# Performance work log

Hardware: AMD Instinct MI355X
Metric: run time of the kernel (lower is better)

Reference implementation:

```python
import jax, jax.numpy as jnp
import numpy as np

N_NODES = 50000
N_EDGES = 800000
IN_NODE = 16
IN_EDGE = 8
HID = 128
N_LAYERS = 4
LN_EPS = 1e-5


def setup_inputs() -> dict:
    key = jax.random.key(0)
    ks = jax.random.split(key, 16)
    s = lambda k, shape, fan: jax.random.normal(k, shape, jnp.float32) * (1.0 / np.sqrt(fan))
    inp = {
        "x": jax.random.normal(ks[0], (N_NODES, IN_NODE), jnp.float32),
        "edge_index": jax.random.randint(ks[1], (2, N_EDGES), 0, N_NODES, jnp.int32),
        "edge_attr": jax.random.normal(ks[2], (N_EDGES, IN_EDGE), jnp.float32),
        # input projection
        "W_in": s(ks[3], (HID, IN_NODE), IN_NODE),
        "b_in": jnp.zeros((HID,), jnp.float32),
        # stacked SAGEConv params: lin_l (neighbors, biased), lin_r (root, no bias)
        "Wl": s(ks[4], (N_LAYERS, HID, HID), HID),
        "bl": jnp.zeros((N_LAYERS, HID), jnp.float32),
        "Wr": s(ks[5], (N_LAYERS, HID, HID), HID),
        # stacked LayerNorm params
        "ln_g": jnp.ones((N_LAYERS, HID), jnp.float32),
        "ln_b": jnp.zeros((N_LAYERS, HID), jnp.float32),
        # edge MLP: (2*HID+IN_EDGE) -> HID -> HID//2 -> 1
        "W1": s(ks[6], (HID, 2 * HID + IN_EDGE), 2 * HID + IN_EDGE),
        "b1": jnp.zeros((HID,), jnp.float32),
        "W2": s(ks[7], (HID // 2, HID), HID),
        "b2": jnp.zeros((HID // 2,), jnp.float32),
        "W3": s(ks[8], (1, HID // 2), HID // 2),
        "b3": jnp.zeros((1,), jnp.float32),
    }
    return inp


def reference(x, edge_index, edge_attr, W_in, b_in, Wl, bl, Wr, ln_g, ln_b, W1, b1, W2, b2, W3, b3):
    n = x.shape[0]
    src, dst = edge_index[0], edge_index[1]
    # in-degree for mean aggregation (clamped to 1, as in PyG mean aggr)
    deg = jax.ops.segment_sum(jnp.ones_like(dst, jnp.float32), dst, num_segments=n)
    deg = jnp.maximum(deg, 1.0)[:, None]  # [N,1]

    h = x @ W_in.T + b_in  # [N,H]

    def layer(h, params):
        Wl_i, bl_i, Wr_i, g_i, be_i = params
        # SAGEConv: mean of source features scattered to destinations
        agg = jax.ops.segment_sum(h[src], dst, num_segments=n) / deg
        h2 = agg @ Wl_i.T + bl_i + h @ Wr_i.T
        # LayerNorm
        mu = jnp.mean(h2, axis=-1, keepdims=True)
        var = jnp.mean(jnp.square(h2 - mu), axis=-1, keepdims=True)
        h2 = (h2 - mu) * jax.lax.rsqrt(var + LN_EPS) * g_i + be_i
        # ReLU (dropout = identity in eval mode)
        return jax.nn.relu(h2), None

    h, _ = jax.lax.scan(layer, h, (Wl, bl, Wr, ln_g, ln_b))

    # edge head: gather endpoints, concat with edge_attr, MLP -> scalar logit
    e = jnp.concatenate([h[src], h[dst], edge_attr], axis=1)  # [E, 2H+F_e]
    e = jax.nn.relu(e @ W1.T + b1)
    e = jax.nn.relu(e @ W2.T + b2)
    logits = (e @ W3.T + b3)[:, 0]  # [E]
    return logits
```

## Files before the change

### kernel.cpp

```cpp
#include <hip/hip_runtime.h>
#include <stdint.h>

#define NN 50000
#define NE 800000

#define O_WIN 0
#define O_BIN 2048
#define O_WL  2176
#define O_BL  67712
#define O_WR  68224
#define O_LNG 133760
#define O_LNB 134272
#define O_W1  134784
#define O_B1  168576
#define O_W2  168704
#define O_B2  176896
#define O_W3  176960
#define O_B3  177024
#define W_TOTAL 177025

#define WS_FLAGS 0
#define WS_WC    512
#define WS_CNT   355072
#define WS_ROWP  555520
#define WS_CUR   756224
#define WS_CSR   956928
#define WS_EID   4156928
#define WS_DST   7356928
#define WS_W1P   10556928
#define WS_HB0   10630656
#define WS_HB1   23430656
#define WS_NEED  36230656

#define SCAN_NB 196

typedef float f32x4 __attribute__((ext_vector_type(4)));
typedef short bf16x8 __attribute__((ext_vector_type(8)));
typedef short bf16x4 __attribute__((ext_vector_type(4)));

__device__ __forceinline__ float b2f(unsigned short u) {
  union { unsigned int i; float f; } v; v.i = ((unsigned int)u) << 16; return v.f;
}
__device__ __forceinline__ unsigned short f2b(float f) {
  union { float f; unsigned int i; } v; v.f = f;
  return (unsigned short)((v.i + 0x7fffu + ((v.i >> 16) & 1u)) >> 16);
}

#define LBAR() do { \
  asm volatile("s_waitcnt lgkmcnt(0)" ::: "memory"); \
  __builtin_amdgcn_s_barrier(); \
} while (0)

__global__ void k_fallback(unsigned short* __restrict__ out) {
  int gid = blockIdx.x * 256 + threadIdx.x;
  if (gid < NE) out[gid] = 0x3F00;
}

__global__ void k_probe(const unsigned short* __restrict__ x_u,
                        const int* __restrict__ ei32, int* __restrict__ flags) {
  const int t = threadIdx.x;
  int insane = 0;
  for (int i = t; i < 512; i += 64) {
    float v = b2f(x_u[i]);
    if (!(fabsf(v) < 1e4f)) insane++;
  }
#pragma unroll
  for (int off = 1; off < 64; off <<= 1) insane += __shfl_xor(insane, off, 64);
  int nz = 0;
  for (int i = t; i < 128; i += 64) nz |= (ei32[2 * i + 1] != 0);
  unsigned long long m = __ballot(nz != 0);
  if (t == 0) {
    flags[0] = (insane >= 16) ? 1 : 0;
    flags[1] = (m == 0ULL) ? 1 : 0;
  }
}

__global__ void k_cvt_w(const void* W_in, const void* b_in, const void* Wl,
                        const void* bl, const void* Wr, const void* lng,
                        const void* lnb, const void* W1, const void* b1,
                        const void* W2, const void* b2, const void* W3,
                        const void* b3, unsigned short* __restrict__ wc,
                        const int* __restrict__ flags) {
  const int gid = blockIdx.x * 256 + threadIdx.x;
  if (gid >= W_TOTAL) return;
  const int f32 = flags[0];
  const void* src; int off;
  if      (gid < O_BIN) { src = W_in; off = gid - O_WIN; }
  else if (gid < O_WL)  { src = b_in; off = gid - O_BIN; }
  else if (gid < O_BL)  { src = Wl;   off = gid - O_WL;  }
  else if (gid < O_WR)  { src = bl;   off = gid - O_BL;  }
  else if (gid < O_LNG) { src = Wr;   off = gid - O_WR;  }
  else if (gid < O_LNB) { src = lng;  off = gid - O_LNG; }
  else if (gid < O_W1)  { src = lnb;  off = gid - O_LNB; }
  else if (gid < O_B1)  { src = W1;   off = gid - O_W1;  }
  else if (gid < O_W2)  { src = b1;   off = gid - O_B1;  }
  else if (gid < O_B2)  { src = W2;   off = gid - O_W2;  }
  else if (gid < O_W3)  { src = b2;   off = gid - O_B2;  }
  else if (gid < O_B3)  { src = W3;   off = gid - O_W3;  }
  else                  { src = b3;   off = 0;           }
  wc[gid] = f32 ? f2b(((const float*)src)[off]) : ((const unsigned short*)src)[off];
}

__global__ void k_build_w1p(const unsigned short* __restrict__ wc,
                            unsigned short* __restrict__ W1p) {
  int gid = blockIdx.x * 256 + threadIdx.x;
  if (gid >= 128 * 288) return;
  int j = gid / 288, k = gid - j * 288;
  W1p[gid] = (k < 264) ? wc[O_W1 + j * 264 + k] : (unsigned short)0;
}

__global__ void k_cvt_ea(const void* __restrict__ ea,
                         unsigned short* __restrict__ eab,
                         const int* __restrict__ flags) {
  const int gid = blockIdx.x * 256 + threadIdx.x;
  if (gid >= NE) return;
  if (flags[0]) {
    const float4* ep = (const float4*)((const float*)ea + (size_t)gid * 8);
    const float4 a = ep[0], b = ep[1];
    union { ushort4 v[2]; int4 i; } o;
    o.v[0].x = f2b(a.x); o.v[0].y = f2b(a.y); o.v[0].z = f2b(a.z); o.v[0].w = f2b(a.w);
    o.v[1].x = f2b(b.x); o.v[1].y = f2b(b.y); o.v[1].z = f2b(b.z); o.v[1].w = f2b(b.w);
    *(int4*)(eab + (size_t)gid * 8) = o.i;
  } else {
    *(int4*)(eab + (size_t)gid * 8) =
        *(const int4*)((const unsigned short*)ea + (size_t)gid * 8);
  }
}

__global__ void k_hist(const int* __restrict__ ei, int* __restrict__ cnt,
                       const int* __restrict__ flags) {
  const int e = blockIdx.x * 256 + threadIdx.x;
  if (e >= NE) return;
  const int d = flags[1] ? ei[2 * (NE + e)] : ei[NE + e];
  atomicAdd(&cnt[d], 1);
}

__global__ __launch_bounds__(256) void k_scan1(const int* __restrict__ cnt,
                                               int* __restrict__ rowptr,
                                               int* __restrict__ bsum) {
  __shared__ int ws4[4];
  const int t = threadIdx.x, ln = t & 63, wv = t >> 6;
  const int i = blockIdx.x * 256 + t;
  const int v = (i < NN) ? cnt[i] : 0;
  int x = v;
#pragma unroll
  for (int off = 1; off < 64; off <<= 1) {
    int y = __shfl_up(x, off, 64);
    if (ln >= off) x += y;
  }
  if (ln == 63) ws4[wv] = x;
  __syncthreads();
  if (t == 0) { ws4[1] += ws4[0]; ws4[2] += ws4[1]; ws4[3] += ws4[2]; }
  __syncthreads();
  const int woff = wv ? ws4[wv - 1] : 0;
  if (i < NN) rowptr[i] = woff + x - v;
  if (t == 255) bsum[blockIdx.x] = woff + x;
}

__global__ __launch_bounds__(256) void k_scan2(int* __restrict__ bsum) {
  __shared__ int ws4[4];
  const int t = threadIdx.x, ln = t & 63, wv = t >> 6;
  const int v = (t < SCAN_NB) ? bsum[t] : 0;
  int x = v;
#pragma unroll
  for (int off = 1; off < 64; off <<= 1) {
    int y = __shfl_up(x, off, 64);
    if (ln >= off) x += y;
  }
  if (ln == 63) ws4[wv] = x;
  __syncthreads();
  if (t == 0) { ws4[1] += ws4[0]; ws4[2] += ws4[1]; ws4[3] += ws4[2]; }
  __syncthreads();
  const int woff = wv ? ws4[wv - 1] : 0;
  if (t < SCAN_NB) bsum[t] = woff + x - v;
}

__global__ void k_scan3(int* __restrict__ rowptr, const int* __restrict__ bsum) {
  const int i = blockIdx.x * 256 + threadIdx.x;
  if (i < NN) rowptr[i] += bsum[blockIdx.x];
  if (i == 0) rowptr[NN] = NE;
}

__global__ void k_fill(const int* __restrict__ ei, const int* __restrict__ rowptr,
                       int* __restrict__ cursor, int* __restrict__ csr,
                       int* __restrict__ eidA, int* __restrict__ dstA,
                       const int* __restrict__ flags) {
  const int e = blockIdx.x * 256 + threadIdx.x;
  if (e >= NE) return;
  const int i64 = flags[1];
  const int s = i64 ? ei[2 * e] : ei[e];
  const int d = i64 ? ei[2 * (NE + e)] : ei[NE + e];
  const int pos = rowptr[d] + atomicAdd(&cursor[d], 1);
  csr[pos] = s;
  eidA[pos] = e;
  dstA[pos] = d;
}

__global__ void k_inproj(const void* __restrict__ x,
                         const unsigned short* __restrict__ wc,
                         unsigned short* __restrict__ hb,
                         const int* __restrict__ flags) {
  const int gid = blockIdx.x * 256 + threadIdx.x;
  const int n = gid >> 7, j = gid & 127;
  float xv[16];
  if (flags[0]) {
    const float4* xp = (const float4*)((const float*)x + (size_t)n * 16);
#pragma unroll
    for (int q = 0; q < 4; q++) {
      float4 t = xp[q];
      xv[q * 4 + 0] = t.x; xv[q * 4 + 1] = t.y; xv[q * 4 + 2] = t.z; xv[q * 4 + 3] = t.w;
    }
  } else {
    const unsigned short* xu = (const unsigned short*)x + (size_t)n * 16;
#pragma unroll
    for (int q = 0; q < 2; q++) {
      union { int4 v; unsigned short u[8]; } t;
      t.v = *(const int4*)(xu + q * 8);
#pragma unroll
      for (int i = 0; i < 8; i++) xv[q * 8 + i] = b2f(t.u[i]);
    }
  }
  float s = b2f(wc[O_BIN + j]);
  const unsigned short* wrow = wc + O_WIN + j * 16;
#pragma unroll
  for (int q = 0; q < 2; q++) {
    union { int4 v; unsigned short u[8]; } w;
    w.v = *(const int4*)(wrow + q * 8);
#pragma unroll
    for (int i = 0; i < 8; i++) s += b2f(w.u[i]) * xv[q * 8 + i];
  }
  hb[gid] = f2b(s);
}

__global__ __launch_bounds__(256) void k_agg(
    const unsigned short* __restrict__ hin, const int* __restrict__ csr,
    const int* __restrict__ rowptr, unsigned short* __restrict__ aggb) {
  const int tid = threadIdx.x;
  const int n = blockIdx.x * 4 + (tid >> 6);
  const int L = tid & 63;
  const int rs = rowptr[n], re = rowptr[n + 1];
  const unsigned int* hw = (const unsigned int*)hin;
  long long t0 = 0, t1 = 0;
  int e = rs;
  for (; e + 8 <= re; e += 8) {
    unsigned int u[8];
#pragma unroll
    for (int k = 0; k < 8; k++) u[k] = hw[(size_t)csr[e + k] * 64 + L];
#pragma unroll
    for (int k = 0; k < 8; k++) {
      t0 += (int)(b2f((unsigned short)(u[k] & 0xffff)) * 16777216.0f);
      t1 += (int)(b2f((unsigned short)(u[k] >> 16)) * 16777216.0f);
    }
  }
  for (; e + 2 <= re; e += 2) {
    const unsigned int u0 = hw[(size_t)csr[e] * 64 + L];
    const unsigned int u1 = hw[(size_t)csr[e + 1] * 64 + L];
    t0 += (int)(b2f((unsigned short)(u0 & 0xffff)) * 16777216.0f);
    t1 += (int)(b2f((unsigned short)(u0 >> 16)) * 16777216.0f);
    t0 += (int)(b2f((unsigned short)(u1 & 0xffff)) * 16777216.0f);
    t1 += (int)(b2f((unsigned short)(u1 >> 16)) * 16777216.0f);
  }
  if (e < re) {
    const unsigned int u0 = hw[(size_t)csr[e] * 64 + L];
    t0 += (int)(b2f((unsigned short)(u0 & 0xffff)) * 16777216.0f);
    t1 += (int)(b2f((unsigned short)(u0 >> 16)) * 16777216.0f);
  }
  const int dg = re - rs;
  const float rd = (1.0f / 16777216.0f) / (float)(dg > 1 ? dg : 1);
  const float s0 = (float)t0 * rd;
  const float s1 = (float)t1 * rd;
  const unsigned int o = (unsigned int)f2b(s0) | ((unsigned int)f2b(s1) << 16);
  ((unsigned int*)aggb)[(size_t)n * 64 + L] = o;
}

__global__ __launch_bounds__(256) void k_sage_mfma(
    const unsigned short* __restrict__ hin, unsigned short* __restrict__ hagg,
    const unsigned short* __restrict__ wc, int l) {
  __shared__ __align__(16) unsigned char As[64 * 528];
  __shared__ float red1[64][4];
  __shared__ float red2[64][4];
  __shared__ float mr[64][2];
  const int tid = threadIdx.x;
  const int wv = tid >> 6;
  const int L = tid & 63;
  const int l15 = L & 15;
  const int q = L >> 4;
  const int n0 = blockIdx.x * 64;

  bf16x8 wf[2][8];
  float blv[2], gv[2], bv[2];
#pragma unroll
  for (int nt = 0; nt < 2; nt++) {
    const int jj = (wv * 2 + nt) * 16 + l15;
#pragma unroll
    for (int kc = 0; kc < 8; kc++) {
      const unsigned short* src = (kc < 4)
          ? wc + O_WL + ((size_t)l * 128 + jj) * 128 + kc * 32 + q * 8
          : wc + O_WR + ((size_t)l * 128 + jj) * 128 + (kc - 4) * 32 + q * 8;
      wf[nt][kc] = *(const bf16x8*)src;
    }
    blv[nt] = b2f(wc[O_BL + l * 128 + jj]);
    gv[nt]  = b2f(wc[O_LNG + l * 128 + jj]);
    bv[nt]  = b2f(wc[O_LNB + l * 128 + jj]);
  }

  for (int c = tid; c < 2048; c += 256) {
    const int row = c >> 5, part = c & 31;
    int node = n0 + row; if (node > NN - 1) node = NN - 1;
    const unsigned short* src = (part < 16)
        ? hagg + (size_t)node * 128 + part * 8
        : hin + (size_t)node * 128 + (part - 16) * 8;
    *(int4*)(As + row * 528 + part * 16) = *(const int4*)src;
  }
  __syncthreads();

  f32x4 acc[4][2];
#pragma unroll
  for (int mt = 0; mt < 4; mt++)
#pragma unroll
    for (int nt = 0; nt < 2; nt++) acc[mt][nt] = (f32x4)(0.0f);
#pragma unroll
  for (int kc = 0; kc < 8; kc++) {
#pragma unroll
    for (int mt = 0; mt < 4; mt++) {
      const bf16x8 a = *(const bf16x8*)(As + (mt * 16 + l15) * 528 + (kc * 32 + q * 8) * 2);
#pragma unroll
      for (int nt = 0; nt < 2; nt++)
        acc[mt][nt] = __builtin_amdgcn_mfma_f32_16x16x32_bf16(a, wf[nt][kc], acc[mt][nt], 0, 0, 0);
    }
  }
#pragma unroll
  for (int mt = 0; mt < 4; mt++) {
#pragma unroll
    for (int rg = 0; rg < 4; rg++) {
      acc[mt][0][rg] += blv[0];
      acc[mt][1][rg] += blv[1];
      float s = acc[mt][0][rg] + acc[mt][1][rg];
      float s2 = acc[mt][0][rg] * acc[mt][0][rg] + acc[mt][1][rg] * acc[mt][1][rg];
#pragma unroll
      for (int m = 1; m < 16; m <<= 1) {
        s += __shfl_xor(s, m, 64);
        s2 += __shfl_xor(s2, m, 64);
      }
      if (l15 == 0) {
        const int row = mt * 16 + q * 4 + rg;
        red1[row][wv] = s; red2[row][wv] = s2;
      }
    }
  }
  __syncthreads();
  if (tid < 64) {
    const float s1 = red1[tid][0] + red1[tid][1] + red1[tid][2] + red1[tid][3];
    const float s2 = red2[tid][0] + red2[tid][1] + red2[tid][2] + red2[tid][3];
    const float mu = s1 * 0.0078125f;
    const float var = s2 * 0.0078125f - mu * mu;
    mr[tid][0] = mu;
    mr[tid][1] = rsqrtf(var + 1e-5f);
  }
  __syncthreads();
#pragma unroll
  for (int mt = 0; mt < 4; mt++) {
#pragma unroll
    for (int rg = 0; rg < 4; rg++) {
      const int row = mt * 16 + q * 4 + rg;
      const int node = n0 + row;
      if (node < NN) {
        const float mu = mr[row][0], rstd = mr[row][1];
#pragma unroll
        for (int nt = 0; nt < 2; nt++) {
          const float o = (acc[mt][nt][rg] - mu) * rstd * gv[nt] + bv[nt];
          hagg[(size_t)node * 128 + (wv * 2 + nt) * 16 + l15] = f2b(fmaxf(o, 0.f));
        }
      }
    }
  }
}

__global__ __launch_bounds__(256) void k_edge_mfma(
    const unsigned short* __restrict__ hb, const int* __restrict__ csr,
    const int* __restrict__ eidA, const int* __restrict__ dstA,
    const unsigned short* __restrict__ eab, const unsigned short* __restrict__ W1p,
    const unsigned short* __restrict__ wc, void* __restrict__ out,
    const int* __restrict__ flags) {
  __shared__ __align__(16) unsigned char sm[47616];
  unsigned char* const Ue = sm;
  unsigned char* const Hs = sm + 4096;
  unsigned char* const E1 = sm + 4096;
  unsigned char* const Ds = sm + 21504;
  unsigned char* const E2 = sm + 38912;
  const int tid = threadIdx.x;
  const int wv = tid >> 6;
  const int L = tid & 63;
  const int l15 = L & 15;
  const int q = L >> 4;
  const int f32 = flags[0];
  const int r4 = tid >> 2, seg = tid & 3;

  for (int i = tid; i < 64 * 12; i += 256)
    *(int*)(Ue + (i / 12) * 64 + 16 + (i % 12) * 4) = 0;

  bf16x8 w1f[2][9];
  float b1v[2];
#pragma unroll
  for (int nt = 0; nt < 2; nt++) {
    const int jj = (wv * 2 + nt) * 16 + l15;
#pragma unroll
    for (int cc = 0; cc < 9; cc++)
      w1f[nt][cc] = *(const bf16x8*)(W1p + jj * 288 + cc * 32 + q * 8);
    b1v[nt] = b2f(wc[O_B1 + jj]);
  }
  bf16x8 w2f[4];
  const int jj2 = wv * 16 + l15;
#pragma unroll
  for (int kc = 0; kc < 4; kc++)
    w2f[kc] = *(const bf16x8*)(wc + O_W2 + jj2 * 128 + kc * 32 + q * 8);
  const float b2v = b2f(wc[O_B2 + jj2]);
  const float b3f = b2f(wc[O_B3]);

  const int NT = NE / 64;

  int4 hsr0, hsr1, hsr2, hsr3;
  int4 dsr0, dsr1, dsr2, dsr3;
  int4 uer; uer.x = uer.y = uer.z = uer.w = 0;
  {
    const int p0 = blockIdx.x * 64;
    const int s0 = csr[p0 + r4];
    const int d0 = dstA[p0 + r4];
    const unsigned short* gs = hb + (size_t)s0 * 128 + seg * 32;
    const unsigned short* gd = hb + (size_t)d0 * 128 + seg * 32;
    hsr0 = ((const int4*)gs)[0]; hsr1 = ((const int4*)gs)[1];
    hsr2 = ((const int4*)gs)[2]; hsr3 = ((const int4*)gs)[3];
    dsr0 = ((const int4*)gd)[0]; dsr1 = ((const int4*)gd)[1];
    dsr2 = ((const int4*)gd)[2]; dsr3 = ((const int4*)gd)[3];
    if (tid < 64) {
      const int e0 = eidA[p0 + tid];
      uer = *(const int4*)(eab + (size_t)e0 * 8);
    }
  }

  for (int t = blockIdx.x; t < NT; t += gridDim.x) {
    const int pbase = t * 64;
    const int tn = (t + (int)gridDim.x < NT) ? (t + (int)gridDim.x) : t;
    const int pnext = tn * 64;

    if (tid < 64) *(int4*)(Ue + tid * 64) = uer;
    {
      unsigned char* ldst = Hs + r4 * 272 + seg * 64;
      ((int4*)ldst)[0] = hsr0; ((int4*)ldst)[1] = hsr1;
      ((int4*)ldst)[2] = hsr2; ((int4*)ldst)[3] = hsr3;
      unsigned char* ldd = Ds + r4 * 272 + seg * 64;
      ((int4*)ldd)[0] = dsr0; ((int4*)ldd)[1] = dsr1;
      ((int4*)ldd)[2] = dsr2; ((int4*)ldd)[3] = dsr3;
    }
    const int sN = csr[pnext + r4];
    const int dN = dstA[pnext + r4];
    int eN = 0;
    if (tid < 64) eN = eidA[pnext + tid];

    LBAR();

    int4 h0, h1, h2, h3, d0, d1, d2, d3;
    {
      const unsigned short* gsn = hb + (size_t)sN * 128 + seg * 32;
      h0 = ((const int4*)gsn)[0]; h1 = ((const int4*)gsn)[1];
      h2 = ((const int4*)gsn)[2]; h3 = ((const int4*)gsn)[3];
      const unsigned short* gdn = hb + (size_t)dN * 128 + seg * 32;
      d0 = ((const int4*)gdn)[0]; d1 = ((const int4*)gdn)[1];
      d2 = ((const int4*)gdn)[2]; d3 = ((const int4*)gdn)[3];
    }
    int4 uen; uen.x = uen.y = uen.z = uen.w = 0;
    if (tid < 64) uen = *(const int4*)(eab + (size_t)eN * 8);

    f32x4 acc1[4][2];
#pragma unroll
    for (int mt = 0; mt < 4; mt++)
#pragma unroll
      for (int nt = 0; nt < 2; nt++) acc1[mt][nt] = (f32x4)(0.0f);
#pragma unroll
    for (int cc = 0; cc < 4; cc++) {
#pragma unroll
      for (int mt = 0; mt < 4; mt++) {
        const bf16x8 a = *(const bf16x8*)(Hs + (mt * 16 + l15) * 272 + (cc * 32 + q * 8) * 2);
#pragma unroll
        for (int nt = 0; nt < 2; nt++)
          acc1[mt][nt] = __builtin_amdgcn_mfma_f32_16x16x32_bf16(a, w1f[nt][cc], acc1[mt][nt], 0, 0, 0);
      }
    }
#pragma unroll
    for (int cc = 4; cc < 8; cc++) {
#pragma unroll
      for (int mt = 0; mt < 4; mt++) {
        const bf16x8 a = *(const bf16x8*)(Ds + (mt * 16 + l15) * 272 + ((cc - 4) * 32 + q * 8) * 2);
#pragma unroll
        for (int nt = 0; nt < 2; nt++)
          acc1[mt][nt] = __builtin_amdgcn_mfma_f32_16x16x32_bf16(a, w1f[nt][cc], acc1[mt][nt], 0, 0, 0);
      }
    }
#pragma unroll
    for (int mt = 0; mt < 4; mt++) {
      const bf16x8 a = *(const bf16x8*)(Ue + (mt * 16 + l15) * 64 + q * 16);
#pragma unroll
      for (int nt = 0; nt < 2; nt++)
        acc1[mt][nt] = __builtin_amdgcn_mfma_f32_16x16x32_bf16(a, w1f[nt][8], acc1[mt][nt], 0, 0, 0);
    }
    LBAR();

#pragma unroll
    for (int mt = 0; mt < 4; mt++)
#pragma unroll
      for (int nt = 0; nt < 2; nt++)
#pragma unroll
        for (int rg = 0; rg < 4; rg++) {
          const int er = mt * 16 + q * 4 + rg;
          const int jj = (wv * 2 + nt) * 16 + l15;
          *(unsigned short*)(E1 + er * 272 + jj * 2) =
              f2b(fmaxf(acc1[mt][nt][rg] + b1v[nt], 0.f));
        }
    LBAR();

    f32x4 acc2[4];
#pragma unroll
    for (int mt = 0; mt < 4; mt++) acc2[mt] = (f32x4)(0.0f);
#pragma unroll
    for (int kc = 0; kc < 4; kc++) {
#pragma unroll
      for (int mt = 0; mt < 4; mt++) {
        const bf16x8 a = *(const bf16x8*)(E1 + (mt * 16 + l15) * 272 + (kc * 32 + q * 8) * 2);
        acc2[mt] = __builtin_amdgcn_mfma_f32_16x16x32_bf16(a, w2f[kc], acc2[mt], 0, 0, 0);
      }
    }
#pragma unroll
    for (int mt = 0; mt < 4; mt++)
#pragma unroll
      for (int rg = 0; rg < 4; rg++) {
        const int er = mt * 16 + q * 4 + rg;
        *(unsigned short*)(E2 + er * 136 + jj2 * 2) =
            f2b(fmaxf(acc2[mt][rg] + b2v, 0.f));
      }
    LBAR();

    const int el = wv * 16 + l15;
    float acc = 0.f;
#pragma unroll
    for (int i4 = 0; i4 < 4; i4++) {
      const bf16x4 v = *(const bf16x4*)(E2 + el * 136 + q * 32 + i4 * 8);
#pragma unroll
      for (int j = 0; j < 4; j++)
        acc += b2f((unsigned short)v[j]) * b2f(wc[O_W3 + q * 16 + i4 * 4 + j]);
    }
    acc += __shfl_xor(acc, 16, 64);
    acc += __shfl_xor(acc, 32, 64);
    if (q == 0) {
      const int e = eidA[pbase + el];
      const float r = acc + b3f;
      if (f32) ((float*)out)[e] = r;
      else     ((unsigned short*)out)[e] = f2b(r);
    }

    hsr0 = h0; hsr1 = h1; hsr2 = h2; hsr3 = h3;
    dsr0 = d0; dsr1 = d1; dsr2 = d2; dsr3 = d3;
    uer = uen;
  }
}

extern "C" void kernel_launch(void* const* d_in, const int* in_sizes, int n_in,
                              void* d_out, int out_size, void* d_ws, size_t ws_size,
                              hipStream_t stream) {
  const void* x  = d_in[0];
  const int*  ei = (const int*)d_in[1];
  const void* ea = d_in[2];

  char* ws = (char*)d_ws;
  int*            flags  = (int*)(ws + WS_FLAGS);
  unsigned short* wc     = (unsigned short*)(ws + WS_WC);
  int*            cnt    = (int*)(ws + WS_CNT);
  int*            rowptr = (int*)(ws + WS_ROWP);
  int*            cursor = (int*)(ws + WS_CUR);
  int*            csr    = (int*)(ws + WS_CSR);
  int*            eidA   = (int*)(ws + WS_EID);
  int*            dstA   = (int*)(ws + WS_DST);
  unsigned short* W1p    = (unsigned short*)(ws + WS_W1P);
  unsigned short* hb0    = (unsigned short*)(ws + WS_HB0);
  unsigned short* hb1    = (unsigned short*)(ws + WS_HB1);
  int*            bsum   = (int*)(ws + WS_CSR);

  if (ws_size < WS_NEED) {
    k_fallback<<<3125, 256, 0, stream>>>((unsigned short*)d_out);
    return;
  }

  k_probe<<<1, 64, 0, stream>>>((const unsigned short*)x, ei, flags);
  k_cvt_w<<<(W_TOTAL + 255) / 256, 256, 0, stream>>>(
      d_in[3], d_in[4], d_in[5], d_in[6], d_in[7], d_in[8], d_in[9],
      d_in[10], d_in[11], d_in[12], d_in[13], d_in[14], d_in[15], wc, flags);
  k_build_w1p<<<144, 256, 0, stream>>>(wc, W1p);

  hipMemsetAsync(cnt, 0, NN * sizeof(int), stream);
  hipMemsetAsync(cursor, 0, NN * sizeof(int), stream);
  k_hist<<<3125, 256, 0, stream>>>(ei, cnt, flags);
  k_scan1<<<SCAN_NB, 256, 0, stream>>>(cnt, rowptr, bsum);
  k_scan2<<<1, 256, 0, stream>>>(bsum);
  k_scan3<<<SCAN_NB, 256, 0, stream>>>(rowptr, bsum);
  k_fill<<<3125, 256, 0, stream>>>(ei, rowptr, cursor, csr, eidA, dstA, flags);

  k_inproj<<<NN * 128 / 256, 256, 0, stream>>>(x, wc, hb0, flags);

  unsigned short* cur = hb0;
  unsigned short* nxt = hb1;
  for (int l = 0; l < 4; l++) {
    k_agg<<<12500, 256, 0, stream>>>(cur, csr, rowptr, nxt);
    k_sage_mfma<<<782, 256, 0, stream>>>(cur, nxt, wc, l);
    unsigned short* tmp = cur; cur = nxt; nxt = tmp;
  }
  unsigned short* eab = nxt;
  k_cvt_ea<<<3125, 256, 0, stream>>>(ea, eab, flags);
  k_edge_mfma<<<3125, 256, 0, stream>>>(cur, csr, eidA, dstA, eab, W1p, wc, d_out, flags);
}
```

Measured before the change: 584.4 us.

## Use float accumulation in aggregation and remap edge MLP MFMA tiles for packed stores

The neighbor aggregation now accumulates in fp32 directly, extracting bf16 halves with bit masks instead of converting through 64-bit fixed-point integers, and unrolls to 16 gathers per iteration to keep more loads in flight. In the edge MLP, output columns are interleaved so each lane owns two adjacent columns and can write packed 32-bit LDS stores. The second layer is retiled as a 2x2 (row by column) split across waves, so each A fragment read from LDS is reused over two column tiles. Float summation gives up the order-independent determinism the fixed-point sums provided.

```diff
diff --git a/kernel.cpp b/kernel.cpp
--- a/kernel.cpp
+++ b/kernel.cpp
@@ -40,6 +40,9 @@
 
 __device__ __forceinline__ float b2f(unsigned short u) {
   union { unsigned int i; float f; } v; v.i = ((unsigned int)u) << 16; return v.f;
+}
+__device__ __forceinline__ float asf(unsigned int u) {
+  union { unsigned int i; float f; } v; v.i = u; return v.f;
 }
 __device__ __forceinline__ unsigned short f2b(float f) {
   union { float f; unsigned int i; } v; v.f = f;
@@ -240,36 +243,37 @@
   const int L = tid & 63;
   const int rs = rowptr[n], re = rowptr[n + 1];
   const unsigned int* hw = (const unsigned int*)hin;
-  long long t0 = 0, t1 = 0;
+  float s0 = 0.f, s1 = 0.f;
   int e = rs;
-  for (; e + 8 <= re; e += 8) {
-    unsigned int u[8];
-#pragma unroll
-    for (int k = 0; k < 8; k++) u[k] = hw[(size_t)csr[e + k] * 64 + L];
-#pragma unroll
-    for (int k = 0; k < 8; k++) {
-      t0 += (int)(b2f((unsigned short)(u[k] & 0xffff)) * 16777216.0f);
-      t1 += (int)(b2f((unsigned short)(u[k] >> 16)) * 16777216.0f);
-    }
-  }
-  for (; e + 2 <= re; e += 2) {
+  for (; e + 16 <= re; e += 16) {
+    unsigned int u[16];
+#pragma unroll
+    for (int k = 0; k < 16; k++) u[k] = hw[(size_t)csr[e + k] * 64 + L];
+#pragma unroll
+    for (int k = 0; k < 16; k++) {
+      s1 += asf(u[k] & 0xffff0000u);
+      s0 += asf(u[k] << 16);
+    }
+  }
+  for (; e + 4 <= re; e += 4) {
+    unsigned int u[4];
+#pragma unroll
+    for (int k = 0; k < 4; k++) u[k] = hw[(size_t)csr[e + k] * 64 + L];
+#pragma unroll
+    for (int k = 0; k < 4; k++) {
+      s1 += asf(u[k] & 0xffff0000u);
+      s0 += asf(u[k] << 16);
+    }
+  }
+  for (; e < re; e++) {
     const unsigned int u0 = hw[(size_t)csr[e] * 64 + L];
-    const unsigned int u1 = hw[(size_t)csr[e + 1] * 64 + L];
-    t0 += (int)(b2f((unsigned short)(u0 & 0xffff)) * 16777216.0f);
-    t1 += (int)(b2f((unsigned short)(u0 >> 16)) * 16777216.0f);
-    t0 += (int)(b2f((unsigned short)(u1 & 0xffff)) * 16777216.0f);
-    t1 += (int)(b2f((unsigned short)(u1 >> 16)) * 16777216.0f);
-  }
-  if (e < re) {
-    const unsigned int u0 = hw[(size_t)csr[e] * 64 + L];
-    t0 += (int)(b2f((unsigned short)(u0 & 0xffff)) * 16777216.0f);
-    t1 += (int)(b2f((unsigned short)(u0 >> 16)) * 16777216.0f);
+    s1 += asf(u0 & 0xffff0000u);
+    s0 += asf(u0 << 16);
   }
   const int dg = re - rs;
-  const float rd = (1.0f / 16777216.0f) / (float)(dg > 1 ? dg : 1);
-  const float s0 = (float)t0 * rd;
-  const float s1 = (float)t1 * rd;
-  const unsigned int o = (unsigned int)f2b(s0) | ((unsigned int)f2b(s1) << 16);
+  const float rd = 1.0f / (float)(dg > 1 ? dg : 1);
+  const unsigned int o =
+      (unsigned int)f2b(s0 * rd) | ((unsigned int)f2b(s1 * rd) << 16);
   ((unsigned int*)aggb)[(size_t)n * 64 + L] = o;
 }
 
@@ -403,18 +407,24 @@
   float b1v[2];
 #pragma unroll
   for (int nt = 0; nt < 2; nt++) {
-    const int jj = (wv * 2 + nt) * 16 + l15;
+    const int jj = wv * 32 + l15 * 2 + nt;
 #pragma unroll
     for (int cc = 0; cc < 9; cc++)
       w1f[nt][cc] = *(const bf16x8*)(W1p + jj * 288 + cc * 32 + q * 8);
     b1v[nt] = b2f(wc[O_B1 + jj]);
   }
-  bf16x8 w2f[4];
-  const int jj2 = wv * 16 + l15;
-#pragma unroll
-  for (int kc = 0; kc < 4; kc++)
-    w2f[kc] = *(const bf16x8*)(wc + O_W2 + jj2 * 128 + kc * 32 + q * 8);
-  const float b2v = b2f(wc[O_B2 + jj2]);
+  const int r2base = (wv & 1) * 32;
+  const int c2base = (wv >> 1) * 32;
+  bf16x8 w2f[2][4];
+  float b2v[2];
+#pragma unroll
+  for (int nt = 0; nt < 2; nt++) {
+    const int jj = c2base + l15 * 2 + nt;
+#pragma unroll
+    for (int kc = 0; kc < 4; kc++)
+      w2f[nt][kc] = *(const bf16x8*)(wc + O_W2 + jj * 128 + kc * 32 + q * 8);
+    b2v[nt] = b2f(wc[O_B2 + jj]);
+  }
   const float b3f = b2f(wc[O_B3]);
 
   const int NT = NE / 64;
@@ -508,34 +518,41 @@
 #pragma unroll
     for (int mt = 0; mt < 4; mt++)
 #pragma unroll
-      for (int nt = 0; nt < 2; nt++)
-#pragma unroll
-        for (int rg = 0; rg < 4; rg++) {
-          const int er = mt * 16 + q * 4 + rg;
-          const int jj = (wv * 2 + nt) * 16 + l15;
-          *(unsigned short*)(E1 + er * 272 + jj * 2) =
-              f2b(fmaxf(acc1[mt][nt][rg] + b1v[nt], 0.f));
-        }
-    LBAR();
-
-    f32x4 acc2[4];
-#pragma unroll
-    for (int mt = 0; mt < 4; mt++) acc2[mt] = (f32x4)(0.0f);
-#pragma unroll
-    for (int kc = 0; kc < 4; kc++) {
-#pragma unroll
-      for (int mt = 0; mt < 4; mt++) {
-        const bf16x8 a = *(const bf16x8*)(E1 + (mt * 16 + l15) * 272 + (kc * 32 + q * 8) * 2);
-        acc2[mt] = __builtin_amdgcn_mfma_f32_16x16x32_bf16(a, w2f[kc], acc2[mt], 0, 0, 0);
-      }
-    }
-#pragma unroll
-    for (int mt = 0; mt < 4; mt++)
-#pragma unroll
       for (int rg = 0; rg < 4; rg++) {
         const int er = mt * 16 + q * 4 + rg;
-        *(unsigned short*)(E2 + er * 136 + jj2 * 2) =
-            f2b(fmaxf(acc2[mt][rg] + b2v, 0.f));
+        const float v0 = fmaxf(acc1[mt][0][rg] + b1v[0], 0.f);
+        const float v1 = fmaxf(acc1[mt][1][rg] + b1v[1], 0.f);
+        const unsigned int pk =
+            (unsigned int)f2b(v0) | ((unsigned int)f2b(v1) << 16);
+        *(unsigned int*)(E1 + er * 272 + (wv * 32 + l15 * 2) * 2) = pk;
+      }
+    LBAR();
+
+    f32x4 acc2[2][2];
+#pragma unroll
+    for (int mt = 0; mt < 2; mt++)
+#pragma unroll
+      for (int nt = 0; nt < 2; nt++) acc2[mt][nt] = (f32x4)(0.0f);
+#pragma unroll
+    for (int kc = 0; kc < 4; kc++) {
+#pragma unroll
+      for (int mt = 0; mt < 2; mt++) {
+        const bf16x8 a = *(const bf16x8*)(E1 + (r2base + mt * 16 + l15) * 272 + (kc * 32 + q * 8) * 2);
+#pragma unroll
+        for (int nt = 0; nt < 2; nt++)
+          acc2[mt][nt] = __builtin_amdgcn_mfma_f32_16x16x32_bf16(a, w2f[nt][kc], acc2[mt][nt], 0, 0, 0);
+      }
+    }
+#pragma unroll
+    for (int mt = 0; mt < 2; mt++)
+#pragma unroll
+      for (int rg = 0; rg < 4; rg++) {
+        const int er = r2base + mt * 16 + q * 4 + rg;
+        const float v0 = fmaxf(acc2[mt][0][rg] + b2v[0], 0.f);
+        const float v1 = fmaxf(acc2[mt][1][rg] + b2v[1], 0.f);
+        const unsigned int pk =
+            (unsigned int)f2b(v0) | ((unsigned int)f2b(v1) << 16);
+        *(unsigned int*)(E2 + er * 136 + (c2base + l15 * 2) * 2) = pk;
       }
     LBAR();
 
```

Result: no change. 593.3 us (+1.5%).

## Gather four neighbor rows per wavefront with 16-byte loads in mean aggregation

Applied to the files above, without the earlier changes.

The aggregation kernel now splits each 64-lane wavefront into four groups of 16 lanes. Each group fetches a different neighbor's 256-byte bf16 row with int4 loads, so one wavefront covers 16 edges per iteration instead of 8 sequential passes. The four group partial sums are combined with cross-lane shuffles. Accumulation switches from the fixed-point int64 scheme to plain fp32 adds, which cuts ALU work but drops the order-independent exact summation.

```diff
diff --git a/kernel.cpp b/kernel.cpp
--- a/kernel.cpp
+++ b/kernel.cpp
@@ -40,6 +40,9 @@
 
 __device__ __forceinline__ float b2f(unsigned short u) {
   union { unsigned int i; float f; } v; v.i = ((unsigned int)u) << 16; return v.f;
+}
+__device__ __forceinline__ float asf(unsigned int u) {
+  union { unsigned int i; float f; } v; v.i = u; return v.f;
 }
 __device__ __forceinline__ unsigned short f2b(float f) {
   union { float f; unsigned int i; } v; v.f = f;
@@ -238,39 +241,69 @@
   const int tid = threadIdx.x;
   const int n = blockIdx.x * 4 + (tid >> 6);
   const int L = tid & 63;
+  const int rg = L >> 4;
+  const int j  = L & 15;
   const int rs = rowptr[n], re = rowptr[n + 1];
-  const unsigned int* hw = (const unsigned int*)hin;
-  long long t0 = 0, t1 = 0;
+  const int4* hv = (const int4*)hin;
+  float s[8];
+#pragma unroll
+  for (int i = 0; i < 8; i++) s[i] = 0.f;
+
   int e = rs;
-  for (; e + 8 <= re; e += 8) {
-    unsigned int u[8];
-#pragma unroll
-    for (int k = 0; k < 8; k++) u[k] = hw[(size_t)csr[e + k] * 64 + L];
-#pragma unroll
-    for (int k = 0; k < 8; k++) {
-      t0 += (int)(b2f((unsigned short)(u[k] & 0xffff)) * 16777216.0f);
-      t1 += (int)(b2f((unsigned short)(u[k] >> 16)) * 16777216.0f);
-    }
-  }
-  for (; e + 2 <= re; e += 2) {
-    const unsigned int u0 = hw[(size_t)csr[e] * 64 + L];
-    const unsigned int u1 = hw[(size_t)csr[e + 1] * 64 + L];
-    t0 += (int)(b2f((unsigned short)(u0 & 0xffff)) * 16777216.0f);
-    t1 += (int)(b2f((unsigned short)(u0 >> 16)) * 16777216.0f);
-    t0 += (int)(b2f((unsigned short)(u1 & 0xffff)) * 16777216.0f);
-    t1 += (int)(b2f((unsigned short)(u1 >> 16)) * 16777216.0f);
+  for (; e + 16 <= re; e += 16) {
+    int idx[4];
+#pragma unroll
+    for (int k = 0; k < 4; k++) idx[k] = csr[e + k * 4 + rg];
+    int4 u[4];
+#pragma unroll
+    for (int k = 0; k < 4; k++) u[k] = hv[(size_t)idx[k] * 16 + j];
+#pragma unroll
+    for (int k = 0; k < 4; k++) {
+      const unsigned int w0 = (unsigned int)u[k].x, w1 = (unsigned int)u[k].y;
+      const unsigned int w2 = (unsigned int)u[k].z, w3 = (unsigned int)u[k].w;
+      s[0] += asf(w0 << 16); s[1] += asf(w0 & 0xffff0000u);
+      s[2] += asf(w1 << 16); s[3] += asf(w1 & 0xffff0000u);
+      s[4] += asf(w2 << 16); s[5] += asf(w2 & 0xffff0000u);
+      s[6] += asf(w3 << 16); s[7] += asf(w3 & 0xffff0000u);
+    }
   }
   if (e < re) {
-    const unsigned int u0 = hw[(size_t)csr[e] * 64 + L];
-    t0 += (int)(b2f((unsigned short)(u0 & 0xffff)) * 16777216.0f);
-    t1 += (int)(b2f((unsigned short)(u0 >> 16)) * 16777216.0f);
-  }
-  const int dg = re - rs;
-  const float rd = (1.0f / 16777216.0f) / (float)(dg > 1 ? dg : 1);
-  const float s0 = (float)t0 * rd;
-  const float s1 = (float)t1 * rd;
-  const unsigned int o = (unsigned int)f2b(s0) | ((unsigned int)f2b(s1) << 16);
-  ((unsigned int*)aggb)[(size_t)n * 64 + L] = o;
+    int idx[4], ok[4];
+#pragma unroll
+    for (int k = 0; k < 4; k++) {
+      const int ee = e + k * 4 + rg;
+      ok[k] = ee < re;
+      idx[k] = csr[ok[k] ? ee : (re - 1)];
+    }
+    int4 u[4];
+#pragma unroll
+    for (int k = 0; k < 4; k++) u[k] = hv[(size_t)idx[k] * 16 + j];
+#pragma unroll
+    for (int k = 0; k < 4; k++) {
+      if (ok[k]) {
+        const unsigned int w0 = (unsigned int)u[k].x, w1 = (unsigned int)u[k].y;
+        const unsigned int w2 = (unsigned int)u[k].z, w3 = (unsigned int)u[k].w;
+        s[0] += asf(w0 << 16); s[1] += asf(w0 & 0xffff0000u);
+        s[2] += asf(w1 << 16); s[3] += asf(w1 & 0xffff0000u);
+        s[4] += asf(w2 << 16); s[5] += asf(w2 & 0xffff0000u);
+        s[6] += asf(w3 << 16); s[7] += asf(w3 & 0xffff0000u);
+      }
+    }
+  }
+
+#pragma unroll
+  for (int i = 0; i < 8; i++) {
+    s[i] += __shfl_xor(s[i], 16, 64);
+    s[i] += __shfl_xor(s[i], 32, 64);
+  }
+  if (rg == 0) {
+    const int dg = re - rs;
+    const float rd = 1.0f / (float)(dg > 1 ? dg : 1);
+    union { int4 v; unsigned short h[8]; } o;
+#pragma unroll
+    for (int i = 0; i < 8; i++) o.h[i] = f2b(s[i] * rd);
+    ((int4*)aggb)[(size_t)n * 16 + j] = o.v;
+  }
 }
 
 __global__ __launch_bounds__(256) void k_sage_mfma(
```

Result: faster. 558.9 us (-4.4%).
